# Kernel tuning notes

Hardware: AMD Instinct MI355X
Metric: run time of the kernel (lower is better)

The kernel has to match this reference:

```python
import jax, jax.numpy as jnp
import numpy as np

TOKENS, IN_DIM, HID, OUT_DIM = 32768, 256, 1024, 256
N_EXP, TOP_K = 8, 2


def setup_inputs() -> dict:
    key = jax.random.key(0)
    ks = jax.random.split(key, 6)
    s_in = 1.0 / np.sqrt(IN_DIM)
    s_hid = 1.0 / np.sqrt(HID)
    return {
        "x": jax.random.normal(ks[0], (TOKENS, IN_DIM), dtype=jnp.float32),
        "Wg": jax.random.uniform(ks[1], (IN_DIM, N_EXP), jnp.float32, -s_in, s_in),
        "W1": jax.random.uniform(ks[2], (N_EXP, IN_DIM, HID), jnp.float32, -s_in, s_in),
        "b1": jax.random.uniform(ks[3], (N_EXP, HID), jnp.float32, -s_in, s_in),
        "W2": jax.random.uniform(ks[4], (N_EXP, HID, OUT_DIM), jnp.float32, -s_hid, s_hid),
        "b2": jax.random.uniform(ks[5], (N_EXP, OUT_DIM), jnp.float32, -s_hid, s_hid),
    }


def reference(x, Wg, W1, b1, W2, b2):
    # Router: softmax over expert logits, pick top-k, renormalize weights
    logits = x @ Wg                                  # [B, E]
    router_probs = jax.nn.softmax(logits, axis=-1)   # [B, E]
    top_w, top_idx = jax.lax.top_k(router_probs, TOP_K)  # [B, K]
    top_w = top_w / jnp.sum(top_w, axis=-1, keepdims=True)
    # Dense all-expert compute (faithful to the torch.stack over experts)
    h = jax.nn.relu(jnp.einsum("bi,eih->beh", x, W1) + b1[None])   # [B, E, H]
    expert_out = jnp.einsum("beh,eho->beo", h, W2) + b2[None]       # [B, E, O]
    # Gather top-k experts per token and combine
    selected = jnp.take_along_axis(expert_out, top_idx[:, :, None], axis=1)  # [B, K, O]
    output = jnp.sum(selected * top_w[:, :, None], axis=1)                   # [B, O]
    return output, router_probs
```

## Files before the change

kernel.cpp:

```cpp
#include <hip/hip_runtime.h>
#include <hip/hip_bf16.h>
#include <stdint.h>

#define T_TOK 32768
#define IN_D  256
#define HID_D 1024
#define OUT_D 256
#define NE    8
#define BM    64
#define HC    32
#define NCH   (HID_D / HC)

typedef unsigned short u16;
typedef __attribute__((ext_vector_type(8))) __bf16 bf16x8;
typedef __attribute__((ext_vector_type(4))) float f32x4;
typedef __attribute__((ext_vector_type(4))) unsigned int u32x4;
typedef __attribute__((ext_vector_type(2))) unsigned int u32x2;

__device__ __forceinline__ u16 f2bf(float f) {
  unsigned int u = __builtin_bit_cast(unsigned int, f);
  u = (u + 0x7FFFu + ((u >> 16) & 1u)) >> 16;
  return (u16)u;
}

__device__ __forceinline__ void gload_lds16(const u16* g, u16* l) {
  __builtin_amdgcn_global_load_lds(
      (const __attribute__((address_space(1))) unsigned int*)g,
      (__attribute__((address_space(3))) unsigned int*)l, 16, 0, 0);
}

__global__ __launch_bounds__(256) void pack_w1_kernel(const float* __restrict__ W1,
                                                      u16* __restrict__ w1p) {
  int b = blockIdx.x * 4 + (threadIdx.x >> 6);
  int f = b & 15, c = (b >> 4) & 31, e = b >> 9;
  int l = threadIdx.x & 63, l15 = l & 15, l4 = l >> 4;
  int h = c * 32 + (f >> 3) * 16 + l15;
  int k0 = (f & 7) * 32 + l4 * 8;
  unsigned int w[4];
#pragma unroll
  for (int p = 0; p < 4; ++p) {
    u16 a = f2bf(W1[((size_t)e * IN_D + k0 + 2 * p) * HID_D + h]);
    u16 bq = f2bf(W1[((size_t)e * IN_D + k0 + 2 * p + 1) * HID_D + h]);
    w[p] = (unsigned int)a | ((unsigned int)bq << 16);
  }
  *reinterpret_cast<u32x4*>(w1p + (size_t)b * 512 + l * 8) = u32x4{w[0], w[1], w[2], w[3]};
}

__global__ __launch_bounds__(256) void pack_w2_kernel(const float* __restrict__ W2,
                                                      u16* __restrict__ w2p) {
  int b = blockIdx.x * 4 + (threadIdx.x >> 6);
  int f = b & 15, c = (b >> 4) & 31, e = b >> 9;
  int l = threadIdx.x & 63, l15 = l & 15, l4 = l >> 4;
  int o = f * 16 + l15;
  int k0 = c * 32 + l4 * 8;
  unsigned int w[4];
#pragma unroll
  for (int p = 0; p < 4; ++p) {
    u16 a = f2bf(W2[((size_t)e * HID_D + k0 + 2 * p) * OUT_D + o]);
    u16 bq = f2bf(W2[((size_t)e * HID_D + k0 + 2 * p + 1) * OUT_D + o]);
    w[p] = (unsigned int)a | ((unsigned int)bq << 16);
  }
  *reinterpret_cast<u32x4*>(w2p + (size_t)b * 512 + l * 8) = u32x4{w[0], w[1], w[2], w[3]};
}

__global__ __launch_bounds__(256) void router_kernel(
    const float* __restrict__ x, const float* __restrict__ Wg,
    u16* __restrict__ xbf, float* __restrict__ probs, int* __restrict__ counts,
    int* __restrict__ list_tok, float* __restrict__ list_w) {
  __shared__ float wg_s[IN_D * NE];
  __shared__ int lcnt[NE];
  __shared__ int gbase[NE];
  int tid = threadIdx.x;
  for (int i = tid; i < IN_D * NE; i += 256) wg_s[i] = Wg[i];
  if (tid < NE) lcnt[tid] = 0;
  __syncthreads();

  int lane = tid & 63;
  int wave = tid >> 6;
  int q = lane & 3;
  int tk = blockIdx.x * 64 + wave * 16 + (lane >> 2);

  float acc[NE];
#pragma unroll
  for (int e = 0; e < NE; ++e) acc[e] = 0.f;
  const float* xrow = x + (size_t)tk * IN_D;
  u16* xbrow = xbf + (size_t)tk * IN_D;
#pragma unroll
  for (int i = 0; i < 16; ++i) {
    int c = i * 4 + q;
    f32x4 v = *reinterpret_cast<const f32x4*>(xrow + c * 4);
    unsigned int lo = (unsigned int)f2bf(v[0]) | ((unsigned int)f2bf(v[1]) << 16);
    unsigned int hi = (unsigned int)f2bf(v[2]) | ((unsigned int)f2bf(v[3]) << 16);
    *reinterpret_cast<u32x2*>(xbrow + c * 4) = u32x2{lo, hi};
#pragma unroll
    for (int j = 0; j < 4; ++j) {
      const float* wr = &wg_s[(c * 4 + j) * NE];
#pragma unroll
      for (int e = 0; e < NE; ++e) acc[e] = fmaf(v[j], wr[e], acc[e]);
    }
  }
#pragma unroll
  for (int e = 0; e < NE; ++e) {
    acc[e] += __shfl_xor(acc[e], 1);
    acc[e] += __shfl_xor(acc[e], 2);
  }
  float m = acc[0];
#pragma unroll
  for (int e = 1; e < NE; ++e) m = fmaxf(m, acc[e]);
  float p[NE], s = 0.f;
#pragma unroll
  for (int e = 0; e < NE; ++e) { p[e] = expf(acc[e] - m); s += p[e]; }
  float inv = 1.f / s;
#pragma unroll
  for (int e = 0; e < NE; ++e) p[e] *= inv;
  int i0 = 0; float p0 = p[0];
#pragma unroll
  for (int e = 1; e < NE; ++e) if (p[e] > p0) { p0 = p[e]; i0 = e; }
  int i1 = -1; float p1 = -1.f;
#pragma unroll
  for (int e = 0; e < NE; ++e) if (e != i0 && p[e] > p1) { p1 = p[e]; i1 = e; }
  float wsum = p0 + p1;

  int lp0 = 0, lp1 = 0;
  if (q == 0) {
    *reinterpret_cast<f32x4*>(probs + (size_t)tk * NE)     = f32x4{p[0], p[1], p[2], p[3]};
    *reinterpret_cast<f32x4*>(probs + (size_t)tk * NE + 4) = f32x4{p[4], p[5], p[6], p[7]};
    lp0 = atomicAdd(&lcnt[i0], 1);
    lp1 = atomicAdd(&lcnt[i1], 1);
  }
  __syncthreads();
  if (tid < NE) gbase[tid] = atomicAdd(&counts[tid], lcnt[tid]);
  __syncthreads();
  if (q == 0) {
    int e0 = gbase[i0] + lp0;
    list_tok[(size_t)i0 * T_TOK + e0] = tk;
    list_w[(size_t)i0 * T_TOK + e0] = p0 / wsum;
    int e1 = gbase[i1] + lp1;
    list_tok[(size_t)i1 * T_TOK + e1] = tk | (1 << 16);
    list_w[(size_t)i1 * T_TOK + e1] = p1 / wsum;
  }
}

__global__ __launch_bounds__(512, 4) void moe_main_kernel(
    const u16* __restrict__ xbf, const u16* __restrict__ w1p,
    const u16* __restrict__ w2p, const float* __restrict__ b1,
    const float* __restrict__ b2, const int* __restrict__ counts,
    const int* __restrict__ list_tok, const float* __restrict__ list_w,
    u16* __restrict__ part) {
  int e = blockIdx.x & 7;
  int tile = blockIdx.x >> 3;
  int cnt = counts[e];
  int base = tile * BM;
  if (base >= cnt) return;

  __shared__ __align__(16) u16 W1s[2][16 * 512];
  __shared__ __align__(16) u16 Hs[2][4 * 512];
  __shared__ float Bs[HID_D];
  __shared__ int toks[BM];
  __shared__ float gw[BM];

  int tid = threadIdx.x;
  int wave = tid >> 6;
  int lane = tid & 63;
  const int l15 = lane & 15;
  const int l4 = lane >> 4;
  const int hh = wave & 1;
  const int tt = wave >> 1;
  const int wo = wave & 3;
  const int wt = wave >> 2;

  if (tid < BM) {
    int idx = base + tid;
    int tv = 0; float w = 0.f;
    if (idx < cnt) { tv = list_tok[(size_t)e * T_TOK + idx]; w = list_w[(size_t)e * T_TOK + idx]; }
    toks[tid] = tv;
    gw[tid] = w;
  }
#pragma unroll
  for (int j = 0; j < 2; ++j) Bs[tid + j * 512] = b1[(size_t)e * HID_D + tid + j * 512];

  const u16* w1base = w1p + (size_t)e * NCH * 16 * 512;
  const u16* w2base = w2p + (size_t)e * NCH * 16 * 512;

  auto stage = [&](int c, int buf) {
#pragma unroll
    for (int j2 = 0; j2 < 2; ++j2) {
      int f = wave * 2 + j2;
      gload_lds16(w1base + ((size_t)c * 16 + f) * 512 + lane * 8, &W1s[buf][f * 512]);
    }
  };
  auto loadW2 = [&](int c, u32x4* w2r) {
#pragma unroll
    for (int of = 0; of < 4; ++of)
      w2r[of] = *reinterpret_cast<const u32x4*>(
          w2base + ((size_t)c * 16 + wo * 4 + of) * 512 + lane * 8);
  };

  stage(0, 0);
  __syncthreads();

  u32x4 bx[8];
  {
    const u16* xr = xbf + (size_t)(toks[tt * 16 + l15] & 0xFFFF) * IN_D + l4 * 8;
#pragma unroll
    for (int kk = 0; kk < 8; ++kk)
      bx[kk] = __builtin_nontemporal_load(reinterpret_cast<const u32x4*>(xr + kk * 32));
  }

  u32x4 w2r[4];
  f32x4 acc[4][2];
#pragma unroll
  for (int a = 0; a < 4; ++a)
#pragma unroll
    for (int b = 0; b < 2; ++b) acc[a][b] = f32x4{0.f, 0.f, 0.f, 0.f};

  auto p1 = [&](int c, int wb, int hb) {
    f32x4 accH = f32x4{0.f, 0.f, 0.f, 0.f};
    __builtin_amdgcn_s_setprio(1);
#pragma unroll
    for (int kk = 0; kk < 8; ++kk) {
      const char* pa = reinterpret_cast<const char*>(&W1s[wb][0]) +
                       (hh * 8 + kk) * 1024 + lane * 16;
      bf16x8 a = __builtin_bit_cast(bf16x8, *reinterpret_cast<const u32x4*>(pa));
      accH = __builtin_amdgcn_mfma_f32_16x16x32_bf16(a, __builtin_bit_cast(bf16x8, bx[kk]), accH, 0, 0, 0);
    }
    __builtin_amdgcn_s_setprio(0);
    f32x4 bias = *reinterpret_cast<const f32x4*>(&Bs[c * HC + hh * 16 + l4 * 4]);
    u16 q0 = f2bf(fmaxf(accH[0] + bias[0], 0.f));
    u16 q1 = f2bf(fmaxf(accH[1] + bias[1], 0.f));
    u16 q2 = f2bf(fmaxf(accH[2] + bias[2], 0.f));
    u16 q3 = f2bf(fmaxf(accH[3] + bias[3], 0.f));
    unsigned int lo = (unsigned int)q0 | ((unsigned int)q1 << 16);
    unsigned int hi = (unsigned int)q2 | ((unsigned int)q3 << 16);
    char* p = reinterpret_cast<char*>(&Hs[hb][0]) + tt * 1024 +
              ((hh * 2 + (l4 >> 1)) * 16 + l15) * 16 + (l4 & 1) * 8;
    *reinterpret_cast<u32x2*>(p) = u32x2{lo, hi};
  };

  auto p2 = [&](int hb) {
    bf16x8 bh[2];
#pragma unroll
    for (int tf = 0; tf < 2; ++tf)
      bh[tf] = __builtin_bit_cast(bf16x8, *reinterpret_cast<const u32x4*>(
          reinterpret_cast<const char*>(&Hs[hb][0]) + (wt * 2 + tf) * 1024 + lane * 16));
    __builtin_amdgcn_s_setprio(1);
#pragma unroll
    for (int of = 0; of < 4; ++of) {
      bf16x8 a = __builtin_bit_cast(bf16x8, w2r[of]);
#pragma unroll
      for (int tf = 0; tf < 2; ++tf)
        acc[of][tf] = __builtin_amdgcn_mfma_f32_16x16x32_bf16(a, bh[tf], acc[of][tf], 0, 0, 0);
    }
    __builtin_amdgcn_s_setprio(0);
  };

  loadW2(0, w2r);
  p1(0, 0, 0);
  stage(1, 1);
  asm volatile("s_waitcnt vmcnt(0) lgkmcnt(0)" ::: "memory");
  __builtin_amdgcn_s_barrier();

#pragma unroll 1
  for (int c = 1; c < NCH; c += 2) {
    if (c + 1 < NCH) stage(c + 1, 0);
    p2(0);
    loadW2(c, w2r);
    p1(c, 1, 1);
    asm volatile("s_waitcnt vmcnt(0) lgkmcnt(0)" ::: "memory");
    __builtin_amdgcn_s_barrier();
    if (c + 1 < NCH) {
      if (c + 2 < NCH) stage(c + 2, 1);
      p2(1);
      loadW2(c + 1, w2r);
      p1(c + 1, 0, 0);
      asm volatile("s_waitcnt vmcnt(0) lgkmcnt(0)" ::: "memory");
      __builtin_amdgcn_s_barrier();
    }
  }
  p2(1);

#pragma unroll
  for (int of = 0; of < 4; ++of) {
    int ob = (wo * 4 + of) * 16 + l4 * 4;
    f32x4 bv = *reinterpret_cast<const f32x4*>(b2 + (size_t)e * OUT_D + ob);
#pragma unroll
    for (int tf = 0; tf < 2; ++tf) {
      int trow = (wt * 2 + tf) * 16 + l15;
      if (base + trow < cnt) {
        int tv = toks[trow];
        int tok = tv & 0xFFFF;
        int slot = tv >> 16;
        float w = gw[trow];
        u16 q0 = f2bf(w * (acc[of][tf][0] + bv[0]));
        u16 q1 = f2bf(w * (acc[of][tf][1] + bv[1]));
        u16 q2 = f2bf(w * (acc[of][tf][2] + bv[2]));
        u16 q3 = f2bf(w * (acc[of][tf][3] + bv[3]));
        unsigned int lo = (unsigned int)q0 | ((unsigned int)q1 << 16);
        unsigned int hi = (unsigned int)q2 | ((unsigned int)q3 << 16);
        u32x2 o2{lo, hi};
        __builtin_nontemporal_store(
            o2, reinterpret_cast<u32x2*>(part + ((size_t)slot * T_TOK + tok) * OUT_D + ob));
      }
    }
  }
}

__global__ __launch_bounds__(256) void combine_kernel(const u16* __restrict__ part,
                                                      float* __restrict__ out) {
  size_t i = (size_t)blockIdx.x * 256 + threadIdx.x;
  u32x4 a = __builtin_nontemporal_load(reinterpret_cast<const u32x4*>(part) + i);
  u32x4 b = __builtin_nontemporal_load(
      reinterpret_cast<const u32x4*>(part + (size_t)T_TOK * OUT_D) + i);
  f32x4 o0, o1;
#pragma unroll
  for (int j = 0; j < 4; ++j) {
    unsigned int ua = a[j], ub = b[j];
    float a0 = __builtin_bit_cast(float, (ua & 0xFFFFu) << 16);
    float a1 = __builtin_bit_cast(float, ua & 0xFFFF0000u);
    float b0 = __builtin_bit_cast(float, (ub & 0xFFFFu) << 16);
    float b1 = __builtin_bit_cast(float, ub & 0xFFFF0000u);
    if (j < 2) { o0[j * 2] = a0 + b0; o0[j * 2 + 1] = a1 + b1; }
    else       { o1[(j - 2) * 2] = a0 + b0; o1[(j - 2) * 2 + 1] = a1 + b1; }
  }
  f32x4* dst = reinterpret_cast<f32x4*>(out) + i * 2;
  __builtin_nontemporal_store(o0, dst);
  __builtin_nontemporal_store(o1, dst + 1);
}

extern "C" void kernel_launch(void* const* d_in, const int* in_sizes, int n_in,
                              void* d_out, int out_size, void* d_ws, size_t ws_size,
                              hipStream_t stream) {
  const float* x  = (const float*)d_in[0];
  const float* Wg = (const float*)d_in[1];
  const float* W1 = (const float*)d_in[2];
  const float* b1 = (const float*)d_in[3];
  const float* W2 = (const float*)d_in[4];
  const float* b2 = (const float*)d_in[5];
  float* out = (float*)d_out;

  char* ws = (char*)d_ws;
  constexpr size_t OFF_XBF  = 0;
  constexpr size_t OFF_W1P  = (size_t)T_TOK * IN_D * 2;
  constexpr size_t OFF_W2P  = OFF_W1P + (size_t)NE * HID_D * IN_D * 2;
  constexpr size_t OFF_CNT  = OFF_W2P + (size_t)NE * OUT_D * HID_D * 2;
  constexpr size_t OFF_LTOK = OFF_CNT + 128;
  constexpr size_t OFF_LW   = OFF_LTOK + (size_t)NE * T_TOK * 4;
  constexpr size_t OFF_PART = OFF_LW + (size_t)NE * T_TOK * 4;

  u16*   xbf      = (u16*)(ws + OFF_XBF);
  u16*   w1p      = (u16*)(ws + OFF_W1P);
  u16*   w2p      = (u16*)(ws + OFF_W2P);
  int*   counts   = (int*)(ws + OFF_CNT);
  int*   list_tok = (int*)(ws + OFF_LTOK);
  float* list_w   = (float*)(ws + OFF_LW);
  u16*   part     = (u16*)(ws + OFF_PART);
  float* probs    = out + (size_t)T_TOK * OUT_D;

  hipMemsetAsync(counts, 0, NE * sizeof(int), stream);

  pack_w1_kernel<<<NE * NCH * 16 / 4, 256, 0, stream>>>(W1, w1p);
  pack_w2_kernel<<<NE * NCH * 16 / 4, 256, 0, stream>>>(W2, w2p);
  router_kernel<<<T_TOK / 64, 256, 0, stream>>>(x, Wg, xbf, probs, counts,
                                                list_tok, list_w);

  moe_main_kernel<<<(T_TOK / BM) * NE, 512, 0, stream>>>(
      xbf, w1p, w2p, b1, b2, counts, list_tok, list_w, part);

  combine_kernel<<<(T_TOK * OUT_D / 8) / 256, 256, 0, stream>>>(part, out);
}
```

Before: 171.1 us.

## Deepen W1 LDS pipeline to four buffers and double-buffer W2 registers

Widens the W1 LDS ring from two to four stages so chunks are prefetched two iterations ahead, and waits with vmcnt(4) instead of draining all loads at each barrier. W2 fragments are double-buffered in registers (w2A/w2B), loaded one chunk early so the second GEMM overlaps with the next loads. The phase-2 work split changes so each wave owns two output fragments across all four token rows, and the s_setprio hints are removed. The cost is more LDS per block (another 32 KB), which may lower occupancy under the 512x4 launch bound, plus a more intricate vmcnt accounting that must stay correct.

```diff
diff --git a/kernel.cpp b/kernel.cpp
--- a/kernel.cpp
+++ b/kernel.cpp
@@ -153,7 +153,7 @@
   int base = tile * BM;
   if (base >= cnt) return;
 
-  __shared__ __align__(16) u16 W1s[2][16 * 512];
+  __shared__ __align__(16) u16 W1s[4][16 * 512];
   __shared__ __align__(16) u16 Hs[2][4 * 512];
   __shared__ float Bs[HID_D];
   __shared__ int toks[BM];
@@ -166,8 +166,6 @@
   const int l4 = lane >> 4;
   const int hh = wave & 1;
   const int tt = wave >> 1;
-  const int wo = wave & 3;
-  const int wt = wave >> 2;
 
   if (tid < BM) {
     int idx = base + tid;
@@ -191,12 +189,13 @@
   };
   auto loadW2 = [&](int c, u32x4* w2r) {
 #pragma unroll
-    for (int of = 0; of < 4; ++of)
+    for (int of = 0; of < 2; ++of)
       w2r[of] = *reinterpret_cast<const u32x4*>(
-          w2base + ((size_t)c * 16 + wo * 4 + of) * 512 + lane * 8);
+          w2base + ((size_t)c * 16 + wave * 2 + of) * 512 + lane * 8);
   };
 
   stage(0, 0);
+  stage(1, 1);
   __syncthreads();
 
   u32x4 bx[8];
@@ -207,16 +206,15 @@
       bx[kk] = __builtin_nontemporal_load(reinterpret_cast<const u32x4*>(xr + kk * 32));
   }
 
-  u32x4 w2r[4];
-  f32x4 acc[4][2];
-#pragma unroll
-  for (int a = 0; a < 4; ++a)
-#pragma unroll
-    for (int b = 0; b < 2; ++b) acc[a][b] = f32x4{0.f, 0.f, 0.f, 0.f};
+  u32x4 w2A[2], w2B[2];
+  f32x4 acc[2][4];
+#pragma unroll
+  for (int a = 0; a < 2; ++a)
+#pragma unroll
+    for (int b = 0; b < 4; ++b) acc[a][b] = f32x4{0.f, 0.f, 0.f, 0.f};
 
   auto p1 = [&](int c, int wb, int hb) {
     f32x4 accH = f32x4{0.f, 0.f, 0.f, 0.f};
-    __builtin_amdgcn_s_setprio(1);
 #pragma unroll
     for (int kk = 0; kk < 8; ++kk) {
       const char* pa = reinterpret_cast<const char*>(&W1s[wb][0]) +
@@ -224,7 +222,6 @@
       bf16x8 a = __builtin_bit_cast(bf16x8, *reinterpret_cast<const u32x4*>(pa));
       accH = __builtin_amdgcn_mfma_f32_16x16x32_bf16(a, __builtin_bit_cast(bf16x8, bx[kk]), accH, 0, 0, 0);
     }
-    __builtin_amdgcn_s_setprio(0);
     f32x4 bias = *reinterpret_cast<const f32x4*>(&Bs[c * HC + hh * 16 + l4 * 4]);
     u16 q0 = f2bf(fmaxf(accH[0] + bias[0], 0.f));
     u16 q1 = f2bf(fmaxf(accH[1] + bias[1], 0.f));
@@ -237,55 +234,67 @@
     *reinterpret_cast<u32x2*>(p) = u32x2{lo, hi};
   };
 
-  auto p2 = [&](int hb) {
-    bf16x8 bh[2];
-#pragma unroll
-    for (int tf = 0; tf < 2; ++tf)
+  auto p2 = [&](int hb, const u32x4* w2r) {
+    bf16x8 bh[4];
+#pragma unroll
+    for (int tf = 0; tf < 4; ++tf)
       bh[tf] = __builtin_bit_cast(bf16x8, *reinterpret_cast<const u32x4*>(
-          reinterpret_cast<const char*>(&Hs[hb][0]) + (wt * 2 + tf) * 1024 + lane * 16));
-    __builtin_amdgcn_s_setprio(1);
-#pragma unroll
-    for (int of = 0; of < 4; ++of) {
+          reinterpret_cast<const char*>(&Hs[hb][0]) + tf * 1024 + lane * 16));
+#pragma unroll
+    for (int of = 0; of < 2; ++of) {
       bf16x8 a = __builtin_bit_cast(bf16x8, w2r[of]);
 #pragma unroll
-      for (int tf = 0; tf < 2; ++tf)
+      for (int tf = 0; tf < 4; ++tf)
         acc[of][tf] = __builtin_amdgcn_mfma_f32_16x16x32_bf16(a, bh[tf], acc[of][tf], 0, 0, 0);
     }
-    __builtin_amdgcn_s_setprio(0);
   };
 
-  loadW2(0, w2r);
-  p1(0, 0, 0);
-  stage(1, 1);
-  asm volatile("s_waitcnt vmcnt(0) lgkmcnt(0)" ::: "memory");
-  __builtin_amdgcn_s_barrier();
+  loadW2(0, w2A);
 
 #pragma unroll 1
-  for (int c = 1; c < NCH; c += 2) {
-    if (c + 1 < NCH) stage(c + 1, 0);
-    p2(0);
-    loadW2(c, w2r);
-    p1(c, 1, 1);
-    asm volatile("s_waitcnt vmcnt(0) lgkmcnt(0)" ::: "memory");
-    __builtin_amdgcn_s_barrier();
-    if (c + 1 < NCH) {
-      if (c + 2 < NCH) stage(c + 2, 1);
-      p2(1);
-      loadW2(c + 1, w2r);
-      p1(c + 1, 0, 0);
-      asm volatile("s_waitcnt vmcnt(0) lgkmcnt(0)" ::: "memory");
+  for (int c = 0; c < NCH; c += 4) {
+    { int j = c + 0;
+      if (j + 2 < NCH) stage(j + 2, 2);
+      if (j > 0) p2(1, w2B);
+      if (j + 1 < NCH) loadW2(j + 1, w2B);
+      p1(j, 0, 0);
+      asm volatile("s_waitcnt vmcnt(4) lgkmcnt(0)" ::: "memory");
       __builtin_amdgcn_s_barrier();
     }
-  }
-  p2(1);
-
-#pragma unroll
-  for (int of = 0; of < 4; ++of) {
-    int ob = (wo * 4 + of) * 16 + l4 * 4;
+    { int j = c + 1;
+      if (j + 2 < NCH) stage(j + 2, 3);
+      p2(0, w2A);
+      if (j + 1 < NCH) loadW2(j + 1, w2A);
+      p1(j, 1, 1);
+      asm volatile("s_waitcnt vmcnt(4) lgkmcnt(0)" ::: "memory");
+      __builtin_amdgcn_s_barrier();
+    }
+    { int j = c + 2;
+      if (j + 2 < NCH) stage(j + 2, 0);
+      p2(1, w2B);
+      if (j + 1 < NCH) loadW2(j + 1, w2B);
+      p1(j, 2, 0);
+      asm volatile("s_waitcnt vmcnt(4) lgkmcnt(0)" ::: "memory");
+      __builtin_amdgcn_s_barrier();
+    }
+    { int j = c + 3;
+      if (j + 2 < NCH) stage(j + 2, 1);
+      p2(0, w2A);
+      if (j + 1 < NCH) loadW2(j + 1, w2A);
+      p1(j, 3, 1);
+      asm volatile("s_waitcnt vmcnt(4) lgkmcnt(0)" ::: "memory");
+      __builtin_amdgcn_s_barrier();
+    }
+  }
+  p2(1, w2B);
+
+#pragma unroll
+  for (int of = 0; of < 2; ++of) {
+    int ob = (wave * 2 + of) * 16 + l4 * 4;
     f32x4 bv = *reinterpret_cast<const f32x4*>(b2 + (size_t)e * OUT_D + ob);
 #pragma unroll
-    for (int tf = 0; tf < 2; ++tf) {
-      int trow = (wt * 2 + tf) * 16 + l15;
+    for (int tf = 0; tf < 4; ++tf) {
+      int trow = tf * 16 + l15;
       if (base + trow < cnt) {
         int tv = toks[trow];
         int tok = tv & 0xFFFF;
```

Measured after the change: 171.2 us. Within noise of the previous version (+0.1%).

## Double-buffer W2 register loads, merge weight pack kernels, drop setprio

Applied to the files above, without the earlier changes.

The W2 fragments are now held in two register sets (w2A/w2B) and loaded one chunk ahead, so the global load for chunk c+1 overlaps the MFMA work of chunk c instead of being issued just before use. The two weight-packing kernels are merged into one launch to save a kernel launch. The s_setprio hints around the MFMA loops are removed. Holding a second W2 fragment set raises register use, which may lower occupancy.

```diff
diff --git a/kernel.cpp b/kernel.cpp
--- a/kernel.cpp
+++ b/kernel.cpp
@@ -29,38 +29,38 @@
       (__attribute__((address_space(3))) unsigned int*)l, 16, 0, 0);
 }
 
-__global__ __launch_bounds__(256) void pack_w1_kernel(const float* __restrict__ W1,
-                                                      u16* __restrict__ w1p) {
-  int b = blockIdx.x * 4 + (threadIdx.x >> 6);
-  int f = b & 15, c = (b >> 4) & 31, e = b >> 9;
+__global__ __launch_bounds__(256) void pack_w_kernel(const float* __restrict__ W1,
+                                                     const float* __restrict__ W2,
+                                                     u16* __restrict__ w1p,
+                                                     u16* __restrict__ w2p) {
+  int gb = blockIdx.x * 4 + (threadIdx.x >> 6);
   int l = threadIdx.x & 63, l15 = l & 15, l4 = l >> 4;
-  int h = c * 32 + (f >> 3) * 16 + l15;
-  int k0 = (f & 7) * 32 + l4 * 8;
   unsigned int w[4];
-#pragma unroll
-  for (int p = 0; p < 4; ++p) {
-    u16 a = f2bf(W1[((size_t)e * IN_D + k0 + 2 * p) * HID_D + h]);
-    u16 bq = f2bf(W1[((size_t)e * IN_D + k0 + 2 * p + 1) * HID_D + h]);
-    w[p] = (unsigned int)a | ((unsigned int)bq << 16);
-  }
-  *reinterpret_cast<u32x4*>(w1p + (size_t)b * 512 + l * 8) = u32x4{w[0], w[1], w[2], w[3]};
-}
-
-__global__ __launch_bounds__(256) void pack_w2_kernel(const float* __restrict__ W2,
-                                                      u16* __restrict__ w2p) {
-  int b = blockIdx.x * 4 + (threadIdx.x >> 6);
-  int f = b & 15, c = (b >> 4) & 31, e = b >> 9;
-  int l = threadIdx.x & 63, l15 = l & 15, l4 = l >> 4;
-  int o = f * 16 + l15;
-  int k0 = c * 32 + l4 * 8;
-  unsigned int w[4];
-#pragma unroll
-  for (int p = 0; p < 4; ++p) {
-    u16 a = f2bf(W2[((size_t)e * HID_D + k0 + 2 * p) * OUT_D + o]);
-    u16 bq = f2bf(W2[((size_t)e * HID_D + k0 + 2 * p + 1) * OUT_D + o]);
-    w[p] = (unsigned int)a | ((unsigned int)bq << 16);
-  }
-  *reinterpret_cast<u32x4*>(w2p + (size_t)b * 512 + l * 8) = u32x4{w[0], w[1], w[2], w[3]};
+  if (gb < NE * NCH * 16) {
+    int b = gb;
+    int f = b & 15, c = (b >> 4) & 31, e = b >> 9;
+    int h = c * 32 + (f >> 3) * 16 + l15;
+    int k0 = (f & 7) * 32 + l4 * 8;
+#pragma unroll
+    for (int p = 0; p < 4; ++p) {
+      u16 a = f2bf(W1[((size_t)e * IN_D + k0 + 2 * p) * HID_D + h]);
+      u16 bq = f2bf(W1[((size_t)e * IN_D + k0 + 2 * p + 1) * HID_D + h]);
+      w[p] = (unsigned int)a | ((unsigned int)bq << 16);
+    }
+    *reinterpret_cast<u32x4*>(w1p + (size_t)b * 512 + l * 8) = u32x4{w[0], w[1], w[2], w[3]};
+  } else {
+    int b = gb - NE * NCH * 16;
+    int f = b & 15, c = (b >> 4) & 31, e = b >> 9;
+    int o = f * 16 + l15;
+    int k0 = c * 32 + l4 * 8;
+#pragma unroll
+    for (int p = 0; p < 4; ++p) {
+      u16 a = f2bf(W2[((size_t)e * HID_D + k0 + 2 * p) * OUT_D + o]);
+      u16 bq = f2bf(W2[((size_t)e * HID_D + k0 + 2 * p + 1) * OUT_D + o]);
+      w[p] = (unsigned int)a | ((unsigned int)bq << 16);
+    }
+    *reinterpret_cast<u32x4*>(w2p + (size_t)b * 512 + l * 8) = u32x4{w[0], w[1], w[2], w[3]};
+  }
 }
 
 __global__ __launch_bounds__(256) void router_kernel(
@@ -207,7 +207,7 @@
       bx[kk] = __builtin_nontemporal_load(reinterpret_cast<const u32x4*>(xr + kk * 32));
   }
 
-  u32x4 w2r[4];
+  u32x4 w2A[4], w2B[4];
   f32x4 acc[4][2];
 #pragma unroll
   for (int a = 0; a < 4; ++a)
@@ -216,7 +216,6 @@
 
   auto p1 = [&](int c, int wb, int hb) {
     f32x4 accH = f32x4{0.f, 0.f, 0.f, 0.f};
-    __builtin_amdgcn_s_setprio(1);
 #pragma unroll
     for (int kk = 0; kk < 8; ++kk) {
       const char* pa = reinterpret_cast<const char*>(&W1s[wb][0]) +
@@ -224,7 +223,6 @@
       bf16x8 a = __builtin_bit_cast(bf16x8, *reinterpret_cast<const u32x4*>(pa));
       accH = __builtin_amdgcn_mfma_f32_16x16x32_bf16(a, __builtin_bit_cast(bf16x8, bx[kk]), accH, 0, 0, 0);
     }
-    __builtin_amdgcn_s_setprio(0);
     f32x4 bias = *reinterpret_cast<const f32x4*>(&Bs[c * HC + hh * 16 + l4 * 4]);
     u16 q0 = f2bf(fmaxf(accH[0] + bias[0], 0.f));
     u16 q1 = f2bf(fmaxf(accH[1] + bias[1], 0.f));
@@ -237,13 +235,12 @@
     *reinterpret_cast<u32x2*>(p) = u32x2{lo, hi};
   };
 
-  auto p2 = [&](int hb) {
+  auto p2 = [&](int hb, const u32x4* w2r) {
     bf16x8 bh[2];
 #pragma unroll
     for (int tf = 0; tf < 2; ++tf)
       bh[tf] = __builtin_bit_cast(bf16x8, *reinterpret_cast<const u32x4*>(
           reinterpret_cast<const char*>(&Hs[hb][0]) + (wt * 2 + tf) * 1024 + lane * 16));
-    __builtin_amdgcn_s_setprio(1);
 #pragma unroll
     for (int of = 0; of < 4; ++of) {
       bf16x8 a = __builtin_bit_cast(bf16x8, w2r[of]);
@@ -251,33 +248,33 @@
       for (int tf = 0; tf < 2; ++tf)
         acc[of][tf] = __builtin_amdgcn_mfma_f32_16x16x32_bf16(a, bh[tf], acc[of][tf], 0, 0, 0);
     }
-    __builtin_amdgcn_s_setprio(0);
   };
 
-  loadW2(0, w2r);
+  loadW2(0, w2A);
   p1(0, 0, 0);
   stage(1, 1);
+  loadW2(1, w2B);
   asm volatile("s_waitcnt vmcnt(0) lgkmcnt(0)" ::: "memory");
   __builtin_amdgcn_s_barrier();
 
 #pragma unroll 1
   for (int c = 1; c < NCH; c += 2) {
     if (c + 1 < NCH) stage(c + 1, 0);
-    p2(0);
-    loadW2(c, w2r);
+    p2(0, w2A);
+    if (c + 1 < NCH) loadW2(c + 1, w2A);
     p1(c, 1, 1);
     asm volatile("s_waitcnt vmcnt(0) lgkmcnt(0)" ::: "memory");
     __builtin_amdgcn_s_barrier();
     if (c + 1 < NCH) {
       if (c + 2 < NCH) stage(c + 2, 1);
-      p2(1);
-      loadW2(c + 1, w2r);
+      p2(1, w2B);
+      if (c + 2 < NCH) loadW2(c + 2, w2B);
       p1(c + 1, 0, 0);
       asm volatile("s_waitcnt vmcnt(0) lgkmcnt(0)" ::: "memory");
       __builtin_amdgcn_s_barrier();
     }
   }
-  p2(1);
+  p2(1, w2B);
 
 #pragma unroll
   for (int of = 0; of < 4; ++of) {
@@ -358,8 +355,7 @@
 
   hipMemsetAsync(counts, 0, NE * sizeof(int), stream);
 
-  pack_w1_kernel<<<NE * NCH * 16 / 4, 256, 0, stream>>>(W1, w1p);
-  pack_w2_kernel<<<NE * NCH * 16 / 4, 256, 0, stream>>>(W2, w2p);
+  pack_w_kernel<<<NE * NCH * 16 * 2 / 4, 256, 0, stream>>>(W1, W2, w1p, w2p);
   router_kernel<<<T_TOK / 64, 256, 0, stream>>>(x, Wg, xbf, probs, counts,
                                                 list_tok, list_w);
 
```

Result: slower. 184.7 us (+7.9%).
